# Performance work log

Measured on AMD Instinct MI355X. Metric: run time of the kernel, lower is better.

## Reference

```python
import jax, jax.numpy as jnp
import numpy as np

ALLOWED_BORDER = 0
CLOBBER_POSITIVES = False
NEG_OVERLAP = 0.3
POS_OVERLAP = 0.7
STRIDE = 16


def _mkanchors(ws, hs, cx, cy):
    return np.stack([cx - 0.5 * (ws - 1), cy - 0.5 * (hs - 1),
                     cx + 0.5 * (ws - 1), cy + 0.5 * (hs - 1)], axis=1)


def _base_anchors(base_size=16, ratios=(0.5, 1.0, 2.0), scales=(8, 16, 32)):
    ratios = np.asarray(ratios, dtype=np.float64)
    scales = np.asarray(scales, dtype=np.float64)
    w = h = float(base_size)
    cx = cy = 0.5 * (base_size - 1)
    size = w * h
    ws = np.round(np.sqrt(size / ratios))
    hs = np.round(ws * ratios)
    ratio_anchors = _mkanchors(ws, hs, cx, cy)  # (3,4)
    out = []
    for x1, y1, x2, y2 in ratio_anchors:
        aw = x2 - x1 + 1
        ah = y2 - y1 + 1
        acx = x1 + 0.5 * (aw - 1)
        acy = y1 + 0.5 * (ah - 1)
        out.append(_mkanchors(aw * scales, ah * scales, acx, acy))
    return np.concatenate(out, axis=0).astype(np.float32)  # (9,4)


def _shift(rr, cc, stride):
    # keras_rcnn.backend.shift: grid of shifted base anchors, (rr*cc*9, 4)
    base = _base_anchors()
    sx = np.arange(rr) * stride
    sy = np.arange(cc) * stride
    SX, SY = np.meshgrid(sx, sy)
    shifts = np.stack([SX.ravel(), SY.ravel(), SX.ravel(), SY.ravel()], axis=1).astype(np.float32)
    return jnp.asarray((shifts[:, None, :] + base[None, :, :]).reshape(-1, 4))


def _iou(a, b):
    # pairwise IoU, (A,4) x (G,4) -> (A,G); +1 pixel convention as in keras-rcnn overlap()
    area_a = (a[:, 2] - a[:, 0] + 1.0) * (a[:, 3] - a[:, 1] + 1.0)
    area_b = (b[:, 2] - b[:, 0] + 1.0) * (b[:, 3] - b[:, 1] + 1.0)
    iw = jnp.maximum(jnp.minimum(a[:, None, 2], b[None, :, 2]) - jnp.maximum(a[:, None, 0], b[None, :, 0]) + 1.0, 0.0)
    ih = jnp.maximum(jnp.minimum(a[:, None, 3], b[None, :, 3]) - jnp.maximum(a[:, None, 1], b[None, :, 1]) + 1.0, 0.0)
    inter = iw * ih
    union = jnp.maximum(area_a[:, None] + area_b[None, :] - inter, 1e-8)
    return inter / union


def _bbox_transform(ex, gt):
    ew = ex[:, 2] - ex[:, 0] + 1.0
    eh = ex[:, 3] - ex[:, 1] + 1.0
    ecx = ex[:, 0] + 0.5 * ew
    ecy = ex[:, 1] + 0.5 * eh
    gw = gt[:, 2] - gt[:, 0] + 1.0
    gh = gt[:, 3] - gt[:, 1] + 1.0
    gcx = gt[:, 0] + 0.5 * gw
    gcy = gt[:, 1] + 0.5 * gh
    return jnp.stack([(gcx - ecx) / ew, (gcy - ecy) / eh,
                      jnp.log(gw / ew), jnp.log(gh / eh)], axis=1)


def setup_inputs():
    key = jax.random.key(0)
    k1, k2, k3 = jax.random.split(key, 3)
    rr = cc = 128
    ch = 18  # 2 * 9 anchors
    G = 256
    H = W = 2048.0
    scores = jax.random.normal(k1, (1, rr, cc, ch), dtype=jnp.float32)
    xy = jax.random.uniform(k2, (1, G, 2), minval=0.0, maxval=1700.0)
    wh = jax.random.uniform(k3, (1, G, 2), minval=16.0, maxval=300.0)
    gt_boxes = jnp.concatenate([xy, xy + wh], axis=-1).astype(jnp.float32)
    metadata = jnp.array([[H, W, 1.0]], dtype=jnp.float32)
    return {"scores": scores, "gt_boxes": gt_boxes, "metadata": metadata}


def reference(scores, gt_boxes, metadata):
    meta = metadata[0, :]
    gt = gt_boxes[0]  # (G,4)
    rr, cc, ch = scores.shape[1:]
    anchors = _shift(rr, cc, STRIDE)  # (A,4), A = rr*cc*9
    # inside_image mask (keeps static shapes: mask instead of gather, unmap at end)
    inside = ((anchors[:, 0] >= -ALLOWED_BORDER) & (anchors[:, 1] >= -ALLOWED_BORDER) &
              (anchors[:, 2] < meta[1] + ALLOWED_BORDER) & (anchors[:, 3] < meta[0] + ALLOWED_BORDER))
    overlaps = _iou(anchors, gt)  # (A,G)
    max_overlaps = overlaps.max(axis=1)          # per-anchor best IoU
    argmax_inds = jnp.argmax(overlaps, axis=1)   # per-anchor best gt
    gt_argmax = jnp.argmax(jnp.where(inside[:, None], overlaps, -1.0), axis=0)  # (G,)
    labels = jnp.full((anchors.shape[0],), -1.0, dtype=jnp.float32)
    if not CLOBBER_POSITIVES:
        labels = jnp.where(max_overlaps < NEG_OVERLAP, 0.0, labels)
    # scatter-add trick from keras-rcnn: sets labels[gt_argmax] to 1 (dup indices accumulate)
    labels = labels.at[gt_argmax].add(1.0 - labels[gt_argmax])
    labels = jnp.where(max_overlaps >= POS_OVERLAP, 1.0, labels)
    if CLOBBER_POSITIVES:
        labels = jnp.where(max_overlaps < NEG_OVERLAP, 0.0, labels)
    bbox = _bbox_transform(anchors, gt[argmax_inds])  # (A,4)
    # unmap: outside anchors -> label -1, bbox targets 0
    labels = jnp.where(inside, labels, -1.0)
    bbox = jnp.where(inside[:, None], bbox, 0.0)
    return labels[None, :], bbox[None, :, :]
```

## Files before the change

kernel.cpp:

```cpp
#include <hip/hip_runtime.h>
#include <stdint.h>

#pragma clang fp contract(off)

#define A_TOTAL 147456
#define G 256
#define NANCHOR_BLOCKS 576
#define TOTAL_BLOCKS (NANCHOR_BLOCKS + G)

__constant__ float c_bx1[9] = { -84.f, -176.f, -360.f,  -56.f, -120.f, -248.f,  -36.f,  -80.f, -168.f };
__constant__ float c_by1[9] = { -40.f,  -88.f, -184.f,  -56.f, -120.f, -248.f,  -80.f, -168.f, -344.f };
__constant__ float c_bx2[9] = {  99.f,  191.f,  375.f,   71.f,  135.f,  263.f,   51.f,   95.f,  183.f };
__constant__ float c_by2[9] = {  55.f,  103.f,  199.f,   71.f,  135.f,  263.f,   95.f,  183.f,  359.f };
__constant__ float c_area[9] = { 17664.f, 70656.f, 282624.f, 16384.f, 65536.f, 262144.f, 15488.f, 61952.f, 247808.f };

__device__ __forceinline__ unsigned int fenc(float f) {
    unsigned int u = __float_as_uint(f);
    return (u & 0x80000000u) ? ~u : (u | 0x80000000u);
}

__device__ __forceinline__ unsigned long long shfl_down_u64(unsigned long long v, int off) {
    unsigned int lo = (unsigned int)v;
    unsigned int hi = (unsigned int)(v >> 32);
    lo = __shfl_down(lo, off, 64);
    hi = __shfl_down(hi, off, 64);
    return ((unsigned long long)hi << 32) | lo;
}

__global__ __launch_bounds__(256) void k_fused(
    const float* __restrict__ gt, const float* __restrict__ meta,
    int* __restrict__ win, float* __restrict__ out)
{
    __shared__ float4 sfull[G];
    __shared__ float4 sbox[G];
    __shared__ float  sarea[G];
    __shared__ int    sg[G];
    __shared__ int    wcnt[4], woff[4], sS;
    __shared__ unsigned long long red[4];

    const float H = meta[0], W = meta[1];

    if (blockIdx.x >= NANCHOR_BLOCKS) {
        const int g = blockIdx.x - NANCHOR_BLOCKS;
        const float gx1 = gt[4*g+0], gy1 = gt[4*g+1], gx2 = gt[4*g+2], gy2 = gt[4*g+3];
        const float area_b = (gx2 - gx1 + 1.0f) * (gy2 - gy1 + 1.0f);
        const int tx = threadIdx.x & 15, ty = threadIdx.x >> 4;

        constexpr int ibx1[9] = {-84,-176,-360,-56,-120,-248,-36,-80,-168};
        constexpr int iby1[9] = {-40,-88,-184,-56,-120,-248,-80,-168,-344};
        constexpr int ibx2[9] = { 99, 191, 375, 71, 135, 263, 51, 95, 183};
        constexpr int iby2[9] = { 55, 103, 199, 71, 135, 263, 95, 183, 359};
        constexpr int iarea[9] = {17664,70656,282624,16384,65536,262144,15488,61952,247808};

        unsigned long long best = 0ULL;
        #pragma unroll
        for (int a = 0; a < 9; ++a) {
            const int xlo_in = (-ibx1[a] + 15) >> 4;
            const int ylo_in = (-iby1[a] + 15) >> 4;
            const int xhi_in = (int)floorf((W - 1.0f - (float)ibx2[a]) * 0.0625f);
            const int yhi_in = (int)floorf((H - 1.0f - (float)iby2[a]) * 0.0625f);
            int xlo = max(max((int)floorf((gx1 - (float)ibx2[a]) * 0.0625f) - 1, xlo_in), 0);
            int xhi = min(min((int)floorf((gx2 - (float)ibx1[a]) * 0.0625f) + 1, xhi_in), 127);
            int ylo = max(max((int)floorf((gy1 - (float)iby2[a]) * 0.0625f) - 1, ylo_in), 0);
            int yhi = min(min((int)floorf((gy2 - (float)iby1[a]) * 0.0625f) + 1, yhi_in), 127);
            const float fa = (float)iarea[a];

            for (int iy = ylo + ty; iy <= yhi; iy += 16) {
                const float ay1 = (float)((iy << 4) + iby1[a]);
                const float ay2 = (float)((iy << 4) + iby2[a]);
                float ih = fminf(ay2, gy2) - fmaxf(ay1, gy1) + 1.0f; ih = fmaxf(ih, 0.0f);
                for (int ix = xlo + tx; ix <= xhi; ix += 16) {
                    const float ax1 = (float)((ix << 4) + ibx1[a]);
                    const float ax2 = (float)((ix << 4) + ibx2[a]);
                    bool inside = (ax1 >= 0.0f) & (ay1 >= 0.0f) & (ax2 < W) & (ay2 < H);
                    float iw = fminf(ax2, gx2) - fmaxf(ax1, gx1) + 1.0f; iw = fmaxf(iw, 0.0f);
                    float inter = iw * ih;
                    float uni = fmaxf(fa + area_b - inter, 1e-8f);
                    float iou = inter / uni;
                    float m = inside ? iou : -1.0f;
                    int n = ((iy << 7) + ix) * 9 + a;
                    unsigned long long e = ((unsigned long long)fenc(m) << 32) | (unsigned int)(~n);
                    if (e > best) best = e;
                }
            }
        }
        for (int off = 32; off >= 1; off >>= 1) {
            unsigned long long o = shfl_down_u64(best, off);
            if (o > best) best = o;
        }
        const int wave = threadIdx.x >> 6, lane = threadIdx.x & 63;
        if (lane == 0) red[wave] = best;
        __syncthreads();
        if (threadIdx.x == 0) {
            unsigned long long v = red[0];
            if (red[1] > v) v = red[1];
            if (red[2] > v) v = red[2];
            if (red[3] > v) v = red[3];
            win[g] = (int)(~(unsigned int)(v & 0xffffffffULL));
        }
        return;
    }

    const int tid = threadIdx.x;
    const int n0 = blockIdx.x * 256;

    {
        const int k0 = n0 / 9, k1 = (n0 + 255) / 9;
        int ix_min, ix_max;
        if ((k0 >> 7) == (k1 >> 7)) { ix_min = k0 & 127; ix_max = k1 & 127; }
        else                        { ix_min = 0;        ix_max = 127;      }
        const int iy_min = k0 >> 7, iy_max = k1 >> 7;
        const float bbx1 = (float)(ix_min * 16 - 360 - 4);
        const float bbx2 = (float)(ix_max * 16 + 375 + 4);
        const float bby1 = (float)(iy_min * 16 - 344 - 4);
        const float bby2 = (float)(iy_max * 16 + 359 + 4);

        float4 b = ((const float4*)gt)[tid];
        sfull[tid] = b;
        bool keep = (b.z >= bbx1) & (b.x <= bbx2) & (b.w >= bby1) & (b.y <= bby2);

        unsigned long long m = __ballot(keep);
        const int wave = tid >> 6, lane = tid & 63;
        const int my = __popcll(m & ((1ULL << lane) - 1ULL));
        if (lane == 0) wcnt[wave] = __popcll(m);
        __syncthreads();
        if (tid == 0) {
            int o = 0;
            #pragma unroll
            for (int w = 0; w < 4; ++w) { woff[w] = o; o += wcnt[w]; }
            sS = o;
        }
        __syncthreads();
        if (keep) {
            int p = woff[wave] + my;
            sbox[p] = b;
            sarea[p] = (b.z - b.x + 1.0f) * (b.w - b.y + 1.0f);
            sg[p] = tid;
        }
        __syncthreads();
    }
    const int S = sS;

    const int n = n0 + tid;
    int k = n / 9;
    int a = n - 9 * k;
    float sx = (float)((k & 127) << 4);
    float sy = (float)((k >> 7) << 4);
    float ax1 = sx + c_bx1[a];
    float ay1 = sy + c_by1[a];
    float ax2 = sx + c_bx2[a];
    float ay2 = sy + c_by2[a];
    bool inside = (ax1 >= 0.0f) & (ay1 >= 0.0f) & (ax2 < W) & (ay2 < H);
    float area_a = c_area[a];

    float bestv = -1.0f;
    int barg = 0;
    #pragma unroll 4
    for (int j = 0; j < S; ++j) {
        float4 bb = sbox[j];
        float iw = fminf(ax2, bb.z) - fmaxf(ax1, bb.x) + 1.0f; iw = fmaxf(iw, 0.0f);
        float ih = fminf(ay2, bb.w) - fmaxf(ay1, bb.y) + 1.0f; ih = fmaxf(ih, 0.0f);
        float inter = iw * ih;
        float uni = fmaxf(area_a + sarea[j] - inter, 1e-8f);
        float iou = inter / uni;
        if (iou > bestv) { bestv = iou; barg = sg[j]; }
    }
    if (bestv <= 0.0f) { bestv = 0.0f; barg = 0; }

    float label = -1.0f;
    if (bestv < 0.3f) label = 0.0f;
    if (bestv >= 0.7f) label = 1.0f;
    if (!inside) label = -1.0f;

    float4 gb = sfull[barg];
    float ew = ax2 - ax1 + 1.0f;
    float eh = ay2 - ay1 + 1.0f;
    float ecx = ax1 + 0.5f * ew;
    float ecy = ay1 + 0.5f * eh;
    float gw = gb.z - gb.x + 1.0f;
    float gh = gb.w - gb.y + 1.0f;
    float gcx = gb.x + 0.5f * gw;
    float gcy = gb.y + 0.5f * gh;
    float t0 = (gcx - ecx) / ew;
    float t1 = (gcy - ecy) / eh;
    float t2 = logf(gw / ew);
    float t3 = logf(gh / eh);
    if (!inside) { t0 = 0.0f; t1 = 0.0f; t2 = 0.0f; t3 = 0.0f; }

    out[n] = label;
    ((float4*)(out + A_TOTAL))[n] = make_float4(t0, t1, t2, t3);
}

__global__ __launch_bounds__(256) void k_fix(
    const float* __restrict__ gt, const int* __restrict__ win,
    float* __restrict__ out)
{
    __shared__ float4 sb[G];
    __shared__ float  sa[G];
    __shared__ int    swin[G];
    const int t = threadIdx.x;
    {
        float4 b = ((const float4*)gt)[t];
        sb[t] = b;
        sa[t] = (b.z - b.x + 1.0f) * (b.w - b.y + 1.0f);
        swin[t] = win[t];
    }
    __syncthreads();

    const int idx = swin[t];
    int k = idx / 9;
    int a = idx - 9 * k;
    float sx = (float)((k & 127) << 4);
    float sy = (float)((k >> 7) << 4);
    float ax1 = sx + c_bx1[a];
    float ay1 = sy + c_by1[a];
    float ax2 = sx + c_bx2[a];
    float ay2 = sy + c_by2[a];
    float area_a = c_area[a];

    float mo = -1.0f;
    int cnt = 0;
    #pragma unroll 4
    for (int g = 0; g < G; ++g) {
        float4 bb = sb[g];
        float iw = fminf(ax2, bb.z) - fmaxf(ax1, bb.x) + 1.0f; iw = fmaxf(iw, 0.0f);
        float ih = fminf(ay2, bb.w) - fmaxf(ay1, bb.y) + 1.0f; ih = fmaxf(ih, 0.0f);
        float inter = iw * ih;
        float uni = fmaxf(area_a + sa[g] - inter, 1e-8f);
        float iou = inter / uni;
        mo = fmaxf(mo, iou);
        cnt += (swin[g] == idx);
    }

    float label = -1.0f;
    if (mo < 0.3f) label = 0.0f;
    label = label + (float)cnt * (1.0f - label);
    if (mo >= 0.7f) label = 1.0f;

    out[idx] = label;
}

extern "C" void kernel_launch(void* const* d_in, const int* in_sizes, int n_in,
                              void* d_out, int out_size, void* d_ws, size_t ws_size,
                              hipStream_t stream) {
    const float* gt   = (const float*)d_in[1];
    const float* meta = (const float*)d_in[2];
    float* out = (float*)d_out;
    int* win = (int*)d_ws;

    k_fused<<<TOTAL_BLOCKS, 256, 0, stream>>>(gt, meta, win, out);
    k_fix<<<1, 256, 0, stream>>>(gt, win, out);
}
```

Baseline: 96.03 us.

## Fuse fix-up kernel into main kernel via last-block atomic counter

Merges the single-block fix-up kernel into the main kernel. A global atomic counter and threadfence let the last finishing block perform the per-gt positive-label fix-up, which removes a second kernel launch. It also drops the shared-memory area array, recomputing box areas inline in the IoU loops. The cost is an extra memset launch for the counter, a fence and atomic in every block, and one tail block doing the serial fix-up work.

```diff
diff --git a/kernel.cpp b/kernel.cpp
--- a/kernel.cpp
+++ b/kernel.cpp
@@ -27,24 +27,25 @@
     return ((unsigned long long)hi << 32) | lo;
 }
 
-__global__ __launch_bounds__(256) void k_fused(
+__global__ __launch_bounds__(256) void k_all(
     const float* __restrict__ gt, const float* __restrict__ meta,
-    int* __restrict__ win, float* __restrict__ out)
+    int* __restrict__ win, int* __restrict__ counter,
+    float* __restrict__ out)
 {
     __shared__ float4 sfull[G];
     __shared__ float4 sbox[G];
-    __shared__ float  sarea[G];
     __shared__ int    sg[G];
-    __shared__ int    wcnt[4], woff[4], sS;
+    __shared__ int    wcnt[4], woff[4], sS, slast;
     __shared__ unsigned long long red[4];
 
     const float H = meta[0], W = meta[1];
+    const int tid = threadIdx.x;
 
     if (blockIdx.x >= NANCHOR_BLOCKS) {
         const int g = blockIdx.x - NANCHOR_BLOCKS;
         const float gx1 = gt[4*g+0], gy1 = gt[4*g+1], gx2 = gt[4*g+2], gy2 = gt[4*g+3];
         const float area_b = (gx2 - gx1 + 1.0f) * (gy2 - gy1 + 1.0f);
-        const int tx = threadIdx.x & 15, ty = threadIdx.x >> 4;
+        const int tx = tid & 15, ty = tid >> 4;
 
         constexpr int ibx1[9] = {-84,-176,-360,-56,-120,-248,-36,-80,-168};
         constexpr int iby1[9] = {-40,-88,-184,-56,-120,-248,-80,-168,-344};
@@ -88,126 +89,125 @@
             unsigned long long o = shfl_down_u64(best, off);
             if (o > best) best = o;
         }
-        const int wave = threadIdx.x >> 6, lane = threadIdx.x & 63;
+        const int wave = tid >> 6, lane = tid & 63;
         if (lane == 0) red[wave] = best;
         __syncthreads();
-        if (threadIdx.x == 0) {
+        if (tid == 0) {
             unsigned long long v = red[0];
             if (red[1] > v) v = red[1];
             if (red[2] > v) v = red[2];
             if (red[3] > v) v = red[3];
             win[g] = (int)(~(unsigned int)(v & 0xffffffffULL));
         }
-        return;
-    }
-
-    const int tid = threadIdx.x;
-    const int n0 = blockIdx.x * 256;
+    } else {
+        const int n0 = blockIdx.x * 256;
+
+        {
+            const int k0 = n0 / 9, k1 = (n0 + 255) / 9;
+            int ix_min, ix_max;
+            if ((k0 >> 7) == (k1 >> 7)) { ix_min = k0 & 127; ix_max = k1 & 127; }
+            else                        { ix_min = 0;        ix_max = 127;      }
+            const int iy_min = k0 >> 7, iy_max = k1 >> 7;
+            const float bbx1 = (float)(ix_min * 16 - 360 - 4);
+            const float bbx2 = (float)(ix_max * 16 + 375 + 4);
+            const float bby1 = (float)(iy_min * 16 - 344 - 4);
+            const float bby2 = (float)(iy_max * 16 + 359 + 4);
+
+            float4 b = ((const float4*)gt)[tid];
+            sfull[tid] = b;
+            bool keep = (b.z >= bbx1) & (b.x <= bbx2) & (b.w >= bby1) & (b.y <= bby2);
+
+            unsigned long long m = __ballot(keep);
+            const int wave = tid >> 6, lane = tid & 63;
+            const int my = __popcll(m & ((1ULL << lane) - 1ULL));
+            if (lane == 0) wcnt[wave] = __popcll(m);
+            __syncthreads();
+            if (tid == 0) {
+                int o = 0;
+                #pragma unroll
+                for (int w = 0; w < 4; ++w) { woff[w] = o; o += wcnt[w]; }
+                sS = o;
+            }
+            __syncthreads();
+            if (keep) {
+                int p = woff[wave] + my;
+                sbox[p] = b;
+                sg[p] = tid;
+            }
+            __syncthreads();
+        }
+        const int S = sS;
+
+        const int n = n0 + tid;
+        int k = n / 9;
+        int a = n - 9 * k;
+        float sx = (float)((k & 127) << 4);
+        float sy = (float)((k >> 7) << 4);
+        float ax1 = sx + c_bx1[a];
+        float ay1 = sy + c_by1[a];
+        float ax2 = sx + c_bx2[a];
+        float ay2 = sy + c_by2[a];
+        bool inside = (ax1 >= 0.0f) & (ay1 >= 0.0f) & (ax2 < W) & (ay2 < H);
+        float area_a = c_area[a];
+
+        float bestv = -1.0f;
+        int bj = 0;
+        #pragma unroll 4
+        for (int j = 0; j < S; ++j) {
+            float4 bb = sbox[j];
+            float iw = fminf(ax2, bb.z) - fmaxf(ax1, bb.x) + 1.0f; iw = fmaxf(iw, 0.0f);
+            float ih = fminf(ay2, bb.w) - fmaxf(ay1, bb.y) + 1.0f; ih = fmaxf(ih, 0.0f);
+            float inter = iw * ih;
+            float areab = (bb.z - bb.x + 1.0f) * (bb.w - bb.y + 1.0f);
+            float uni = fmaxf(area_a + areab - inter, 1e-8f);
+            float iou = inter / uni;
+            if (iou > bestv) { bestv = iou; bj = j; }
+        }
+        int barg;
+        if (bestv <= 0.0f) { bestv = 0.0f; barg = 0; }
+        else               { barg = sg[bj]; }
+
+        float label = -1.0f;
+        if (bestv < 0.3f) label = 0.0f;
+        if (bestv >= 0.7f) label = 1.0f;
+        if (!inside) label = -1.0f;
+
+        float4 gb = sfull[barg];
+        float ew = ax2 - ax1 + 1.0f;
+        float eh = ay2 - ay1 + 1.0f;
+        float ecx = ax1 + 0.5f * ew;
+        float ecy = ay1 + 0.5f * eh;
+        float gw = gb.z - gb.x + 1.0f;
+        float gh = gb.w - gb.y + 1.0f;
+        float gcx = gb.x + 0.5f * gw;
+        float gcy = gb.y + 0.5f * gh;
+        float t0 = (gcx - ecx) / ew;
+        float t1 = (gcy - ecy) / eh;
+        float t2 = logf(gw / ew);
+        float t3 = logf(gh / eh);
+        if (!inside) { t0 = 0.0f; t1 = 0.0f; t2 = 0.0f; t3 = 0.0f; }
+
+        out[n] = label;
+        ((float4*)(out + A_TOTAL))[n] = make_float4(t0, t1, t2, t3);
+    }
+
+    __threadfence();
+    __syncthreads();
+    if (tid == 0) {
+        int prev = atomicAdd(counter, 1);
+        slast = (prev == TOTAL_BLOCKS - 1) ? 1 : 0;
+    }
+    __syncthreads();
+    if (slast == 0) return;
 
     {
-        const int k0 = n0 / 9, k1 = (n0 + 255) / 9;
-        int ix_min, ix_max;
-        if ((k0 >> 7) == (k1 >> 7)) { ix_min = k0 & 127; ix_max = k1 & 127; }
-        else                        { ix_min = 0;        ix_max = 127;      }
-        const int iy_min = k0 >> 7, iy_max = k1 >> 7;
-        const float bbx1 = (float)(ix_min * 16 - 360 - 4);
-        const float bbx2 = (float)(ix_max * 16 + 375 + 4);
-        const float bby1 = (float)(iy_min * 16 - 344 - 4);
-        const float bby2 = (float)(iy_max * 16 + 359 + 4);
-
         float4 b = ((const float4*)gt)[tid];
         sfull[tid] = b;
-        bool keep = (b.z >= bbx1) & (b.x <= bbx2) & (b.w >= bby1) & (b.y <= bby2);
-
-        unsigned long long m = __ballot(keep);
-        const int wave = tid >> 6, lane = tid & 63;
-        const int my = __popcll(m & ((1ULL << lane) - 1ULL));
-        if (lane == 0) wcnt[wave] = __popcll(m);
-        __syncthreads();
-        if (tid == 0) {
-            int o = 0;
-            #pragma unroll
-            for (int w = 0; w < 4; ++w) { woff[w] = o; o += wcnt[w]; }
-            sS = o;
-        }
-        __syncthreads();
-        if (keep) {
-            int p = woff[wave] + my;
-            sbox[p] = b;
-            sarea[p] = (b.z - b.x + 1.0f) * (b.w - b.y + 1.0f);
-            sg[p] = tid;
-        }
-        __syncthreads();
-    }
-    const int S = sS;
-
-    const int n = n0 + tid;
-    int k = n / 9;
-    int a = n - 9 * k;
-    float sx = (float)((k & 127) << 4);
-    float sy = (float)((k >> 7) << 4);
-    float ax1 = sx + c_bx1[a];
-    float ay1 = sy + c_by1[a];
-    float ax2 = sx + c_bx2[a];
-    float ay2 = sy + c_by2[a];
-    bool inside = (ax1 >= 0.0f) & (ay1 >= 0.0f) & (ax2 < W) & (ay2 < H);
-    float area_a = c_area[a];
-
-    float bestv = -1.0f;
-    int barg = 0;
-    #pragma unroll 4
-    for (int j = 0; j < S; ++j) {
-        float4 bb = sbox[j];
-        float iw = fminf(ax2, bb.z) - fmaxf(ax1, bb.x) + 1.0f; iw = fmaxf(iw, 0.0f);
-        float ih = fminf(ay2, bb.w) - fmaxf(ay1, bb.y) + 1.0f; ih = fmaxf(ih, 0.0f);
-        float inter = iw * ih;
-        float uni = fmaxf(area_a + sarea[j] - inter, 1e-8f);
-        float iou = inter / uni;
-        if (iou > bestv) { bestv = iou; barg = sg[j]; }
-    }
-    if (bestv <= 0.0f) { bestv = 0.0f; barg = 0; }
-
-    float label = -1.0f;
-    if (bestv < 0.3f) label = 0.0f;
-    if (bestv >= 0.7f) label = 1.0f;
-    if (!inside) label = -1.0f;
-
-    float4 gb = sfull[barg];
-    float ew = ax2 - ax1 + 1.0f;
-    float eh = ay2 - ay1 + 1.0f;
-    float ecx = ax1 + 0.5f * ew;
-    float ecy = ay1 + 0.5f * eh;
-    float gw = gb.z - gb.x + 1.0f;
-    float gh = gb.w - gb.y + 1.0f;
-    float gcx = gb.x + 0.5f * gw;
-    float gcy = gb.y + 0.5f * gh;
-    float t0 = (gcx - ecx) / ew;
-    float t1 = (gcy - ecy) / eh;
-    float t2 = logf(gw / ew);
-    float t3 = logf(gh / eh);
-    if (!inside) { t0 = 0.0f; t1 = 0.0f; t2 = 0.0f; t3 = 0.0f; }
-
-    out[n] = label;
-    ((float4*)(out + A_TOTAL))[n] = make_float4(t0, t1, t2, t3);
-}
-
-__global__ __launch_bounds__(256) void k_fix(
-    const float* __restrict__ gt, const int* __restrict__ win,
-    float* __restrict__ out)
-{
-    __shared__ float4 sb[G];
-    __shared__ float  sa[G];
-    __shared__ int    swin[G];
-    const int t = threadIdx.x;
-    {
-        float4 b = ((const float4*)gt)[t];
-        sb[t] = b;
-        sa[t] = (b.z - b.x + 1.0f) * (b.w - b.y + 1.0f);
-        swin[t] = win[t];
+        sg[tid] = atomicAdd(&win[tid], 0);
     }
     __syncthreads();
 
-    const int idx = swin[t];
+    const int idx = sg[tid];
     int k = idx / 9;
     int a = idx - 9 * k;
     float sx = (float)((k & 127) << 4);
@@ -222,14 +222,15 @@
     int cnt = 0;
     #pragma unroll 4
     for (int g = 0; g < G; ++g) {
-        float4 bb = sb[g];
+        float4 bb = sfull[g];
         float iw = fminf(ax2, bb.z) - fmaxf(ax1, bb.x) + 1.0f; iw = fmaxf(iw, 0.0f);
         float ih = fminf(ay2, bb.w) - fmaxf(ay1, bb.y) + 1.0f; ih = fmaxf(ih, 0.0f);
         float inter = iw * ih;
-        float uni = fmaxf(area_a + sa[g] - inter, 1e-8f);
+        float areab = (bb.z - bb.x + 1.0f) * (bb.w - bb.y + 1.0f);
+        float uni = fmaxf(area_a + areab - inter, 1e-8f);
         float iou = inter / uni;
         mo = fmaxf(mo, iou);
-        cnt += (swin[g] == idx);
+        cnt += (sg[g] == idx);
     }
 
     float label = -1.0f;
@@ -247,7 +248,8 @@
     const float* meta = (const float*)d_in[2];
     float* out = (float*)d_out;
     int* win = (int*)d_ws;
-
-    k_fused<<<TOTAL_BLOCKS, 256, 0, stream>>>(gt, meta, win, out);
-    k_fix<<<1, 256, 0, stream>>>(gt, win, out);
-}
+    int* counter = win + 256;
+
+    hipMemsetAsync(counter, 0, sizeof(int), stream);
+    k_all<<<TOTAL_BLOCKS, 256, 0, stream>>>(gt, meta, win, counter, out);
+}
```

New measurement: 146.4 us. 52.4% more time.

## Tile anchor blocks by aspect and 16x16 spatial tile, skip non-overlapping IoU

Applied to the files above, without the earlier changes.

Anchor blocks now each cover one base anchor shape over a 16x16 spatial tile rather than a contiguous run of flat anchor indices. This makes the per-block gt culling box much tighter, so fewer gt boxes survive into the inner loop. The loop also skips the division when no lane in the wave has overlap, and gt areas are recomputed in registers instead of read from shared memory. The trade-off is strided, non-coalesced output stores, since consecutive threads now write anchors nine entries apart.

```diff
diff --git a/kernel.cpp b/kernel.cpp
--- a/kernel.cpp
+++ b/kernel.cpp
@@ -31,20 +31,20 @@
     const float* __restrict__ gt, const float* __restrict__ meta,
     int* __restrict__ win, float* __restrict__ out)
 {
-    __shared__ float4 sfull[G];
     __shared__ float4 sbox[G];
-    __shared__ float  sarea[G];
     __shared__ int    sg[G];
     __shared__ int    wcnt[4], woff[4], sS;
+    __shared__ float4 sg0;
     __shared__ unsigned long long red[4];
 
     const float H = meta[0], W = meta[1];
+    const int tid = threadIdx.x;
 
     if (blockIdx.x >= NANCHOR_BLOCKS) {
         const int g = blockIdx.x - NANCHOR_BLOCKS;
         const float gx1 = gt[4*g+0], gy1 = gt[4*g+1], gx2 = gt[4*g+2], gy2 = gt[4*g+3];
         const float area_b = (gx2 - gx1 + 1.0f) * (gy2 - gy1 + 1.0f);
-        const int tx = threadIdx.x & 15, ty = threadIdx.x >> 4;
+        const int tx = tid & 15, ty = tid >> 4;
 
         constexpr int ibx1[9] = {-84,-176,-360,-56,-120,-248,-36,-80,-168};
         constexpr int iby1[9] = {-40,-88,-184,-56,-120,-248,-80,-168,-344};
@@ -88,10 +88,10 @@
             unsigned long long o = shfl_down_u64(best, off);
             if (o > best) best = o;
         }
-        const int wave = threadIdx.x >> 6, lane = threadIdx.x & 63;
+        const int wave = tid >> 6, lane = tid & 63;
         if (lane == 0) red[wave] = best;
         __syncthreads();
-        if (threadIdx.x == 0) {
+        if (tid == 0) {
             unsigned long long v = red[0];
             if (red[1] > v) v = red[1];
             if (red[2] > v) v = red[2];
@@ -101,22 +101,24 @@
         return;
     }
 
-    const int tid = threadIdx.x;
-    const int n0 = blockIdx.x * 256;
+    const int a  = blockIdx.x >> 6;
+    const int t  = blockIdx.x & 63;
+    const int ix = ((t & 7) << 4) + (tid & 15);
+    const int iy = ((t >> 3) << 4) + (tid >> 4);
+
+    const float bx1 = c_bx1[a], by1 = c_by1[a], bx2 = c_bx2[a], by2 = c_by2[a];
+    const float area_a = c_area[a];
 
     {
-        const int k0 = n0 / 9, k1 = (n0 + 255) / 9;
-        int ix_min, ix_max;
-        if ((k0 >> 7) == (k1 >> 7)) { ix_min = k0 & 127; ix_max = k1 & 127; }
-        else                        { ix_min = 0;        ix_max = 127;      }
-        const int iy_min = k0 >> 7, iy_max = k1 >> 7;
-        const float bbx1 = (float)(ix_min * 16 - 360 - 4);
-        const float bbx2 = (float)(ix_max * 16 + 375 + 4);
-        const float bby1 = (float)(iy_min * 16 - 344 - 4);
-        const float bby2 = (float)(iy_max * 16 + 359 + 4);
+        const float tx0 = (float)(((t & 7) << 8));
+        const float ty0 = (float)(((t >> 3) << 8));
+        const float bbx1 = tx0 + bx1 - 4.0f;
+        const float bbx2 = tx0 + 240.0f + bx2 + 4.0f;
+        const float bby1 = ty0 + by1 - 4.0f;
+        const float bby2 = ty0 + 240.0f + by2 + 4.0f;
 
         float4 b = ((const float4*)gt)[tid];
-        sfull[tid] = b;
+        if (tid == 0) sg0 = b;
         bool keep = (b.z >= bbx1) & (b.x <= bbx2) & (b.w >= bby1) & (b.y <= bby2);
 
         unsigned long long m = __ballot(keep);
@@ -134,45 +136,42 @@
         if (keep) {
             int p = woff[wave] + my;
             sbox[p] = b;
-            sarea[p] = (b.z - b.x + 1.0f) * (b.w - b.y + 1.0f);
             sg[p] = tid;
         }
         __syncthreads();
     }
     const int S = sS;
 
-    const int n = n0 + tid;
-    int k = n / 9;
-    int a = n - 9 * k;
-    float sx = (float)((k & 127) << 4);
-    float sy = (float)((k >> 7) << 4);
-    float ax1 = sx + c_bx1[a];
-    float ay1 = sy + c_by1[a];
-    float ax2 = sx + c_bx2[a];
-    float ay2 = sy + c_by2[a];
-    bool inside = (ax1 >= 0.0f) & (ay1 >= 0.0f) & (ax2 < W) & (ay2 < H);
-    float area_a = c_area[a];
+    const float ax1 = (float)((ix << 4)) + bx1;
+    const float ay1 = (float)((iy << 4)) + by1;
+    const float ax2 = (float)((ix << 4)) + bx2;
+    const float ay2 = (float)((iy << 4)) + by2;
+    const bool inside = (ax1 >= 0.0f) & (ay1 >= 0.0f) & (ax2 < W) & (ay2 < H);
 
     float bestv = -1.0f;
-    int barg = 0;
-    #pragma unroll 4
+    int bj = 0;
     for (int j = 0; j < S; ++j) {
         float4 bb = sbox[j];
         float iw = fminf(ax2, bb.z) - fmaxf(ax1, bb.x) + 1.0f; iw = fmaxf(iw, 0.0f);
         float ih = fminf(ay2, bb.w) - fmaxf(ay1, bb.y) + 1.0f; ih = fmaxf(ih, 0.0f);
         float inter = iw * ih;
-        float uni = fmaxf(area_a + sarea[j] - inter, 1e-8f);
-        float iou = inter / uni;
-        if (iou > bestv) { bestv = iou; barg = sg[j]; }
-    }
-    if (bestv <= 0.0f) { bestv = 0.0f; barg = 0; }
+        if (__any(inter > 0.0f)) {
+            float areab = (bb.z - bb.x + 1.0f) * (bb.w - bb.y + 1.0f);
+            float uni = fmaxf(area_a + areab - inter, 1e-8f);
+            float iou = inter / uni;
+            if (iou > bestv) { bestv = iou; bj = j; }
+        }
+    }
+    int barg; float4 gb;
+    if (bestv <= 0.0f) { bestv = 0.0f; barg = 0; gb = sg0; }
+    else               { barg = sg[bj]; gb = sbox[bj]; }
+    (void)barg;
 
     float label = -1.0f;
     if (bestv < 0.3f) label = 0.0f;
     if (bestv >= 0.7f) label = 1.0f;
     if (!inside) label = -1.0f;
 
-    float4 gb = sfull[barg];
     float ew = ax2 - ax1 + 1.0f;
     float eh = ay2 - ay1 + 1.0f;
     float ecx = ax1 + 0.5f * ew;
@@ -187,6 +186,7 @@
     float t3 = logf(gh / eh);
     if (!inside) { t0 = 0.0f; t1 = 0.0f; t2 = 0.0f; t3 = 0.0f; }
 
+    const int n = ((iy << 7) + ix) * 9 + a;
     out[n] = label;
     ((float4*)(out + A_TOTAL))[n] = make_float4(t0, t1, t2, t3);
 }
```

New measurement: 90.91 us. -5.3%, faster.
